# Optimization experiments

Hardware: AMD Instinct MI355X
Metric: run time of the kernel (lower is better)

The kernel has to match this reference:

```python
import jax, jax.numpy as jnp
import numpy as np

# dims: P planes, N planar nodes/plane, M nexus nodes, E edges/plane, C classes
P, N, M, E, C, FP, FN = 3, 100000, 30000, 200000, 5, 64, 32


def class_linear(x, W, b):
    # x: [..., C, in], W: [C, out, in], b: [C, out] -> [..., C, out]
    return jnp.einsum('...ci,coi->...co', x, W) + b


def setup_inputs() -> dict:
    key = jax.random.key(0)
    ks = jax.random.split(key, 12)
    def nrm(k, shape, scale=1.0):
        return jax.random.normal(k, shape, jnp.float32) * scale
    return {
        'x': nrm(ks[0], (P, N, C, FP)),
        'nexus': nrm(ks[1], (M, C, FN)),
        'edge_src': jax.random.randint(ks[2], (P, E), 0, N, jnp.int32),
        'edge_dst': jax.random.randint(ks[3], (P, E), 0, M, jnp.int32),
        'Wn1': nrm(ks[4], (C, FN, P * FP), (P * FP) ** -0.5),
        'bn1': jnp.zeros((C, FN), jnp.float32),
        'Wn2': nrm(ks[5], (C, FN, FN), FN ** -0.5),
        'bn2': jnp.zeros((C, FN), jnp.float32),
        'We': nrm(ks[6], (P, C, 1, FP + FN), (FP + FN) ** -0.5),
        'be': jnp.zeros((P, C, 1), jnp.float32),
        'Wd1': nrm(ks[7], (P, C, FP, FP + FN), (FP + FN) ** -0.5),
        'bd1': jnp.zeros((P, C, FP), jnp.float32),
        'Wd2': nrm(ks[8], (P, C, FP, FP), FP ** -0.5),
        'bd2': jnp.zeros((P, C, FP), jnp.float32),
    }


def reference(x, nexus, edge_src, edge_dst, Wn1, bn1, Wn2, bn2,
              We, be, Wd1, bd1, Wd2, bd2):
    # --- nexus_up: SimpleConv (sum-aggregate planar features at nexus nodes) ---
    def up_one(xp, src, dst):
        return jax.ops.segment_sum(xp[src], dst, num_segments=M)  # [M,C,FP]
    up = jax.vmap(up_one)(x, edge_src, edge_dst)                   # [P,M,C,FP]
    # torch.cat(n, dim=-1) over planes -> [M, C, P*FP]
    n_cat = jnp.transpose(up, (1, 2, 0, 3)).reshape(M, C, P * FP)

    # --- nexus_net: ClassLinear -> tanh -> ClassLinear -> tanh ---
    n = jnp.tanh(class_linear(n_cat, Wn1, bn1))
    n = jnp.tanh(class_linear(n, Wn2, bn2))                        # [M,C,FN]

    # --- nexus_down per plane (flow target_to_source, aggr mean at src) ---
    def down_one(xp, src, dst, We_p, be_p, W1, b1, W2, b2):
        x_i = xp[src]                                              # [E,C,FP]
        n_j = n[dst]                                               # [E,C,FN]
        feat = jax.lax.stop_gradient(jnp.concatenate([x_i, n_j], -1))
        # per-class scalar logit, softmax over class dim (dim=1)
        w = jax.nn.softmax(class_linear(feat, We_p, be_p), axis=1)  # [E,C,1]
        msg = w * n_j                                               # [E,C,FN]
        s = jax.ops.segment_sum(msg, src, num_segments=N)           # [N,C,FN]
        cnt = jax.ops.segment_sum(jnp.ones((E,), msg.dtype), src, num_segments=N)
        aggr = s / jnp.maximum(cnt, 1.0)[:, None, None]             # scatter-mean
        h = jnp.tanh(class_linear(jnp.concatenate([xp, aggr], -1), W1, b1))
        return jnp.tanh(class_linear(h, W2, b2))                    # [N,C,FP]

    out = jax.vmap(down_one)(x, edge_src, edge_dst, We, be, Wd1, bd1, Wd2, bd2)
    return out  # [P,N,C,FP] updated planar embeddings (x['u'],x['v'],x['y'])
```

## Files before the change

kernel.cpp:

```cpp
#include <hip/hip_runtime.h>
#include <hip/hip_fp16.h>

#define P_ 3
#define N_ 100000
#define M_ 30000
#define E_ 200000
#define C_ 5
#define FP_ 64
#define FN_ 32
#define PFP_ 192
#define FPFN_ 96
#define PE_ 600000
#define PN_ 300000
#define PM_ 90000
#define NT_ 64
#define TILES_ ((N_ + NT_ - 1) / NT_)
#define NTD_ 128
#define TILESD_ ((N_ + NTD_ - 1) / NTD_)
#define CFN_ 160
#define NW1_ 92160
#define NW2_ 61440
#define NWN1_ 30720
#define NB_S_ ((PN_ + 1023) / 1024)
#define NB_D_ ((PM_ + 1023) / 1024)
#define NB_CNT_ ((PE_ + 255) / 256)
#define NB_WC_ ((NW1_ + 255) / 256)
#define NB_PROJ_ (P_ * TILES_)
#define NB_FILL_ ((PE_ + 255) / 256)

typedef _Float16 f16x8 __attribute__((ext_vector_type(8)));
typedef float f32x4 __attribute__((ext_vector_type(4)));

__device__ __forceinline__ float fast_tanh(float v) {
  float t = __expf(2.0f * v);
  return 1.0f - __fdividef(2.0f, t + 1.0f);
}

__device__ __forceinline__ f16x8 ld8(const __half* p) {
  return *(const f16x8*)(const void*)p;
}

__global__ void k_countw(const int* __restrict__ esrc, const int* __restrict__ edst,
                         int* __restrict__ cnt_src, int* __restrict__ cnt_dst,
                         const float* __restrict__ Wd1, const float* __restrict__ Wd2,
                         const float* __restrict__ Wn1,
                         __half* __restrict__ w1h, __half* __restrict__ w2h,
                         __half* __restrict__ wn1h) {
  int b = blockIdx.x;
  if (b < NB_CNT_) {
    int i = b * 256 + threadIdx.x;
    if (i >= PE_) return;
    int p = i / E_;
    atomicAdd(&cnt_src[p * N_ + esrc[i]], 1);
    atomicAdd(&cnt_dst[p * M_ + edst[i]], 1);
  } else {
    int i = (b - NB_CNT_) * 256 + threadIdx.x;
    if (i < NW1_) w1h[i] = __float2half(Wd1[i]);
    if (i < NW2_) w2h[i] = __float2half(Wd2[i]);
    if (i < NWN1_) wn1h[i] = __float2half(Wn1[i]);
  }
}

__global__ void k_scan1c(const int* __restrict__ in_s, int* __restrict__ out_s,
                         int* __restrict__ aux_s,
                         const int* __restrict__ in_d, int* __restrict__ out_d,
                         int* __restrict__ aux_d) {
  __shared__ int lds[256];
  int b = blockIdx.x, t = threadIdx.x;
  const int* in;
  int* out;
  int* aux;
  int n;
  if (b < NB_S_) { in = in_s; out = out_s; aux = aux_s; n = PN_; }
  else           { b -= NB_S_; in = in_d; out = out_d; aux = aux_d; n = PM_; }
  int base = b * 1024 + t * 4;
  int v0 = (base + 0 < n) ? in[base + 0] : 0;
  int v1 = (base + 1 < n) ? in[base + 1] : 0;
  int v2 = (base + 2 < n) ? in[base + 2] : 0;
  int v3 = (base + 3 < n) ? in[base + 3] : 0;
  lds[t] = v0 + v1 + v2 + v3;
  __syncthreads();
  for (int off = 1; off < 256; off <<= 1) {
    int xv = (t >= off) ? lds[t - off] : 0;
    __syncthreads();
    lds[t] += xv;
    __syncthreads();
  }
  if (t == 255) aux[b] = lds[255];
  int run = (t == 0) ? 0 : lds[t - 1];
  if (base + 0 < n) out[base + 0] = run; run += v0;
  if (base + 1 < n) out[base + 1] = run; run += v1;
  if (base + 2 < n) out[base + 2] = run; run += v2;
  if (base + 3 < n) out[base + 3] = run;
}

__global__ void k_scan2c(int* __restrict__ aux_s, int* __restrict__ end_s,
                         int* __restrict__ aux_d, int* __restrict__ end_d) {
  __shared__ int lds[1024];
  int t = threadIdx.x;
  int* aux = (blockIdx.x == 0) ? aux_s : aux_d;
  int* offe = (blockIdx.x == 0) ? end_s : end_d;
  int nb = (blockIdx.x == 0) ? NB_S_ : NB_D_;
  lds[t] = (t < nb) ? aux[t] : 0;
  __syncthreads();
  for (int off = 1; off < 1024; off <<= 1) {
    int xv = (t >= off) ? lds[t - off] : 0;
    __syncthreads();
    lds[t] += xv;
    __syncthreads();
  }
  if (t < nb) aux[t] = (t == 0) ? 0 : lds[t - 1];
  if (t == 0) offe[0] = lds[nb - 1];
}

__global__ void k_scan3c(int* __restrict__ off_s, const int* __restrict__ aux_s,
                         int* __restrict__ cur_s,
                         int* __restrict__ off_d, const int* __restrict__ aux_d,
                         int* __restrict__ cur_d) {
  int i = blockIdx.x * 256 + threadIdx.x;
  if (i < PN_) {
    int v = off_s[i] + aux_s[i >> 10];
    off_s[i] = v;
    cur_s[i] = v;
  } else if (i < PN_ + PM_) {
    int j = i - PN_;
    int v = off_d[j] + aux_d[j >> 10];
    off_d[j] = v;
    cur_d[j] = v;
  }
}

__global__ __launch_bounds__(256) void k_projfill(
    const float* __restrict__ x, const __half* __restrict__ wn1h,
    const float* __restrict__ We,
    __half* __restrict__ y, float* __restrict__ xdot,
    __half* __restrict__ xh, int write_xh,
    const int* __restrict__ esrc, const int* __restrict__ edst,
    int* __restrict__ cur_src, int* __restrict__ cur_dst,
    int* __restrict__ list_src, int* __restrict__ list_src_e,
    int* __restrict__ list_dst, int* __restrict__ list_dst_e) {
  __shared__ __align__(16) __half xs[NT_ * 320];
  int bp = blockIdx.x;
  int t = threadIdx.x;

  if (bp >= NB_PROJ_) {
    int i = (bp - NB_PROJ_) * 256 + t;
    if (i < PE_) {
      int p = i / E_;
      int s = esrc[i], d = edst[i];
      int ps = atomicAdd(&cur_src[p * N_ + s], 1);
      list_src[ps] = d;
      list_src_e[ps] = i;
      int pd = atomicAdd(&cur_dst[p * M_ + d], 1);
      list_dst[pd] = s;
      list_dst_e[pd] = i;
    }
    return;
  }

  int p = bp / TILES_, tile = bp % TILES_;
  int base = tile * NT_;
  int rows = min(NT_, N_ - base);

  const float* xb = x + (size_t)(p * N_ + base) * 320;
  __half* xo = xh + (size_t)(p * N_ + base) * 320;
  for (int idx = t; idx < rows * 40; idx += 256) {
    int row = idx / 40, col = idx % 40;
    const float4* s4 = (const float4*)&xb[row * 320 + col * 8];
    float4 v0 = s4[0], v1 = s4[1];
    union { __half2 h[4]; float4 f; } u4;
    u4.h[0] = __floats2half2_rn(v0.x, v0.y);
    u4.h[1] = __floats2half2_rn(v0.z, v0.w);
    u4.h[2] = __floats2half2_rn(v1.x, v1.y);
    u4.h[3] = __floats2half2_rn(v1.z, v1.w);
    *(float4*)&xs[row * 320 + ((col * 8) ^ ((row & 7) << 3))] = u4.f;
    if (write_xh) *(float4*)&xo[row * 320 + col * 8] = u4.f;
  }
  __syncthreads();

  int w = t >> 6, l = t & 63;
  int l15 = l & 15, l4 = l >> 4;
  int nA = w * 16 + l15;
  int swzA = (nA & 7) << 3;

  #pragma unroll
  for (int c = 0; c < C_; ++c) {
    f16x8 a0 = ld8(&xs[nA * 320 + ((c * 64 + 0  + l4 * 8) ^ swzA)]);
    f16x8 a1 = ld8(&xs[nA * 320 + ((c * 64 + 32 + l4 * 8) ^ swzA)]);
    #pragma unroll
    for (int ct = 0; ct < 2; ++ct) {
      const __half* wb = &wn1h[(size_t)(c * 32 + ct * 16 + l15) * PFP_ + p * 64];
      f16x8 b0 = ld8(&wb[0  + l4 * 8]);
      f16x8 b1 = ld8(&wb[32 + l4 * 8]);
      f32x4 acc = (f32x4){0.f, 0.f, 0.f, 0.f};
      acc = __builtin_amdgcn_mfma_f32_16x16x32_f16(a0, b0, acc, 0, 0, 0);
      acc = __builtin_amdgcn_mfma_f32_16x16x32_f16(a1, b1, acc, 0, 0, 0);
      #pragma unroll
      for (int r = 0; r < 4; ++r) {
        int node = w * 16 + l4 * 4 + r;
        if (node < rows)
          y[(size_t)(p * N_ + base + node) * CFN_ + c * 32 + ct * 16 + l15] =
              __float2half(acc[r]);
      }
    }
  }

  for (int idx = t; idx < C_ * NT_; idx += 256) {
    int cx = idx >> 6, nodex = idx & 63;
    if (nodex < rows) {
      int swz = (nodex & 7) << 3;
      const float2* wer = (const float2*)&We[(p * C_ + cx) * FPFN_];
      float s = 0.f;
      #pragma unroll
      for (int i = 0; i < 32; ++i) {
        __half2 xv = *(const __half2*)&xs[nodex * 320 + ((cx * 64 + 2 * i) ^ swz)];
        float2 wv = wer[i];
        s += __low2float(xv) * wv.x + __high2float(xv) * wv.y;
      }
      xdot[(size_t)(p * N_ + base + nodex) * C_ + cx] = s;
    }
  }
}

__global__ __launch_bounds__(320) void k_nexus(
    const __half* __restrict__ y,
    const int* __restrict__ off_dst, const int* __restrict__ list_dst,
    const int* __restrict__ list_dst_e, const int* __restrict__ esrc,
    const float* __restrict__ bn1,
    const float* __restrict__ Wn2, const float* __restrict__ bn2,
    const float* __restrict__ We,
    const float* __restrict__ xdot, const float* __restrict__ be,
    __half* __restrict__ nout, __half* __restrict__ wbuf) {
  __shared__ float part[4][CFN_];
  __shared__ __align__(16) float h1S[CFN_];
  __shared__ __align__(16) float h2S[CFN_];
  __shared__ float ndS[P_ * C_];
  __shared__ float beS[P_ * C_];
  int m = blockIdx.x;
  int t = threadIdx.x;
  int g = t / 80, u2 = t % 80;

  float afx = 0.f, afy = 0.f;
  #pragma unroll
  for (int p = 0; p < P_; ++p) {
    int o0 = off_dst[p * M_ + m];
    int o1 = off_dst[p * M_ + m + 1];
    const __half2* yp2 = (const __half2*)(y + (size_t)p * N_ * CFN_);
    for (int e0 = o0 + g; e0 < o1; e0 += 8) {
      int e1 = e0 + 4;
      int s0 = list_dst[e0];
      int s1 = list_dst[e1 < o1 ? e1 : e0];
      __half2 v0 = yp2[(size_t)s0 * 80 + u2];
      __half2 v1 = yp2[(size_t)s1 * 80 + u2];
      afx += __low2float(v0); afy += __high2float(v0);
      if (e1 < o1) { afx += __low2float(v1); afy += __high2float(v1); }
    }
  }
  part[g][2 * u2]     = afx;
  part[g][2 * u2 + 1] = afy;
  __syncthreads();
  if (t < CFN_) {
    float pre = part[0][t] + part[1][t] + part[2][t] + part[3][t] + bn1[t];
    h1S[t] = fast_tanh(pre);
  }
  __syncthreads();
  if (t < CFN_) {
    int c = t >> 5;
    const float4* f4 = (const float4*)&h1S[c * FN_];
    const float4* w4 = (const float4*)&Wn2[(size_t)t * FN_];
    float a = bn2[t];
    #pragma unroll
    for (int i = 0; i < FN_ / 4; ++i) {
      float4 f = f4[i], wv = w4[i];
      a += f.x * wv.x + f.y * wv.y + f.z * wv.z + f.w * wv.w;
    }
    float nv = fast_tanh(a);
    h2S[t] = nv;
    nout[(size_t)m * CFN_ + t] = __float2half(nv);
  }
  __syncthreads();
  if (t < P_ * C_) {
    int p = t / C_, cc = t % C_;
    const float* wv = &We[(p * C_ + cc) * FPFN_ + FP_];
    float a = 0.f;
    #pragma unroll
    for (int j = 0; j < FN_; ++j) a += h2S[cc * FN_ + j] * wv[j];
    ndS[t] = a;
    beS[t] = be[t];
  }
  __syncthreads();
  #pragma unroll
  for (int p = 0; p < P_; ++p) {
    int o0 = off_dst[p * M_ + m];
    int o1 = off_dst[p * M_ + m + 1];
    for (int e = o0 + t; e < o1; e += 320) {
      int i = list_dst_e[e];
      int src = esrc[i];
      const float* xd = &xdot[(size_t)(p * N_ + src) * C_];
      float lg[C_];
      #pragma unroll
      for (int cc = 0; cc < C_; ++cc) lg[cc] = xd[cc] + ndS[p * C_ + cc] + beS[p * C_ + cc];
      float mx = fmaxf(fmaxf(fmaxf(lg[0], lg[1]), fmaxf(lg[2], lg[3])), lg[4]);
      float s = 0.f;
      #pragma unroll
      for (int cc = 0; cc < C_; ++cc) { lg[cc] = __expf(lg[cc] - mx); s += lg[cc]; }
      float inv = __fdividef(1.0f, s);
      __half* wp = &wbuf[(size_t)i * C_];
      #pragma unroll
      for (int cc = 0; cc < C_; ++cc) wp[cc] = __float2half(lg[cc] * inv);
    }
  }
}

template<int XH>
__global__ __launch_bounds__(256, 6) void k_dec(
    const float* __restrict__ x, const __half* __restrict__ xh,
    const __half* __restrict__ nout, const __half* __restrict__ wbuf,
    const int* __restrict__ off_src, const int* __restrict__ list_src,
    const int* __restrict__ list_src_e,
    const __half* __restrict__ w1h, const float* __restrict__ bd1,
    const __half* __restrict__ w2h, const float* __restrict__ bd2,
    float* __restrict__ out) {
  __shared__ __align__(16) __half featS[NTD_ * 104];

  int bp = blockIdx.x;
  int pc = bp / TILESD_;
  int tile = bp % TILESD_;
  int p = pc / C_, c = pc % C_;
  int base = tile * NTD_;
  int rows = min(NTD_, N_ - base);

  int t = threadIdx.x;
  int w = t >> 6, l = t & 63;
  int l15 = l & 15, l4 = l >> 4;

  if constexpr (XH) {
    for (int idx = t; idx < NTD_ * 8; idx += 256) {
      int node = idx >> 3, q = idx & 7;
      if (node < rows) {
        float4 v = *(const float4*)&xh[(size_t)(p * N_ + base + node) * 320 + c * 64 + q * 8];
        *(float4*)&featS[node * 104 + q * 8] = v;
      }
    }
  } else {
    for (int idx = t; idx < NTD_ * 16; idx += 256) {
      int node = idx >> 4, fq = idx & 15;
      if (node < rows) {
        float4 v = *(const float4*)&x[(size_t)(p * N_ + base + node) * 320 + c * 64 + fq * 4];
        __half2* dst = (__half2*)&featS[node * 104 + fq * 4];
        dst[0] = __floats2half2_rn(v.x, v.y);
        dst[1] = __floats2half2_rn(v.z, v.w);
      }
    }
  }
  {
    int nd = t >> 1, hf = t & 1;
    if (nd < rows) {
      int pn = p * N_ + base + nd;
      int o0 = off_src[pn], o1 = off_src[pn + 1];
      __half2 acc[8];
      #pragma unroll
      for (int i = 0; i < 8; ++i) acc[i] = __floats2half2_rn(0.f, 0.f);
      for (int e = o0; e < o1; e += 2) {
        int e1 = e + 1;
        bool has1 = (e1 < o1);
        int d0 = list_src[e];
        int i0 = list_src_e[e];
        int d1 = list_src[has1 ? e1 : e];
        int i1 = list_src_e[has1 ? e1 : e];
        __half wg0h = wbuf[(size_t)i0 * C_ + c];
        __half wg1h = wbuf[(size_t)i1 * C_ + c];
        const __half2* nr0 = (const __half2*)&nout[(size_t)d0 * CFN_ + c * FN_ + hf * 16];
        const __half2* nr1 = (const __half2*)&nout[(size_t)d1 * CFN_ + c * FN_ + hf * 16];
        __half2 v0[8], v1[8];
        #pragma unroll
        for (int i = 0; i < 8; ++i) v0[i] = nr0[i];
        #pragma unroll
        for (int i = 0; i < 8; ++i) v1[i] = nr1[i];
        __half2 wg0 = __half2half2(wg0h);
        #pragma unroll
        for (int i = 0; i < 8; ++i) acc[i] = __hfma2(wg0, v0[i], acc[i]);
        if (has1) {
          __half2 wg1 = __half2half2(wg1h);
          #pragma unroll
          for (int i = 0; i < 8; ++i) acc[i] = __hfma2(wg1, v1[i], acc[i]);
        }
      }
      float invd = __fdividef(1.0f, fmaxf((float)(o1 - o0), 1.0f));
      __half2 invd2 = __float2half2_rn(invd);
      __half2* dst2 = (__half2*)&featS[nd * 104 + 64 + hf * 16];
      #pragma unroll
      for (int i = 0; i < 8; ++i) dst2[i] = __hmul2(acc[i], invd2);
    }
  }
  __syncthreads();

  int rbase = w * 32;
  const __half* w1g = w1h + (size_t)(p * C_ + c) * 64 * 96;
  const __half* w2g = w2h + (size_t)(p * C_ + c) * 64 * 64;

  f32x4 acc[2][4];
  #pragma unroll
  for (int tt = 0; tt < 4; ++tt) {
    float bv = bd1[(p * C_ + c) * FP_ + tt * 16 + l15];
    #pragma unroll
    for (int rt = 0; rt < 2; ++rt) acc[rt][tt] = (f32x4){bv, bv, bv, bv};
  }
  #pragma unroll
  for (int s = 0; s < 3; ++s) {
    f16x8 a0 = ld8(&featS[(rbase + l15) * 104 + s * 32 + l4 * 8]);
    f16x8 a1 = ld8(&featS[(rbase + 16 + l15) * 104 + s * 32 + l4 * 8]);
    #pragma unroll
    for (int tt = 0; tt < 4; ++tt) {
      f16x8 b = ld8(&w1g[(tt * 16 + l15) * 96 + s * 32 + l4 * 8]);
      acc[0][tt] = __builtin_amdgcn_mfma_f32_16x16x32_f16(a0, b, acc[0][tt], 0, 0, 0);
      acc[1][tt] = __builtin_amdgcn_mfma_f32_16x16x32_f16(a1, b, acc[1][tt], 0, 0, 0);
    }
  }
  #pragma unroll
  for (int rt = 0; rt < 2; ++rt)
    #pragma unroll
    for (int tt = 0; tt < 4; ++tt) {
      #pragma unroll
      for (int r = 0; r < 4; ++r) {
        int nrow = rbase + rt * 16 + l4 * 4 + r;
        featS[nrow * 104 + tt * 16 + l15] = __float2half(fast_tanh(acc[rt][tt][r]));
      }
    }

  f32x4 acc2[2][4];
  #pragma unroll
  for (int tt = 0; tt < 4; ++tt) {
    float bv = bd2[(p * C_ + c) * FP_ + tt * 16 + l15];
    #pragma unroll
    for (int rt = 0; rt < 2; ++rt) acc2[rt][tt] = (f32x4){bv, bv, bv, bv};
  }
  #pragma unroll
  for (int s = 0; s < 2; ++s) {
    f16x8 a0 = ld8(&featS[(rbase + l15) * 104 + s * 32 + l4 * 8]);
    f16x8 a1 = ld8(&featS[(rbase + 16 + l15) * 104 + s * 32 + l4 * 8]);
    #pragma unroll
    for (int tt = 0; tt < 4; ++tt) {
      f16x8 b = ld8(&w2g[(tt * 16 + l15) * 64 + s * 32 + l4 * 8]);
      acc2[0][tt] = __builtin_amdgcn_mfma_f32_16x16x32_f16(a0, b, acc2[0][tt], 0, 0, 0);
      acc2[1][tt] = __builtin_amdgcn_mfma_f32_16x16x32_f16(a1, b, acc2[1][tt], 0, 0, 0);
    }
  }
  #pragma unroll
  for (int rt = 0; rt < 2; ++rt)
    #pragma unroll
    for (int tt = 0; tt < 4; ++tt) {
      #pragma unroll
      for (int r = 0; r < 4; ++r) {
        int nrow = rbase + rt * 16 + l4 * 4 + r;
        int node = base + nrow;
        if (node < N_) {
          out[(size_t)(p * N_ + node) * 320 + c * 64 + tt * 16 + l15] =
              fast_tanh(acc2[rt][tt][r]);
        }
      }
    }
}

#define WS_Y      0ll
#define WS_NOUT   24000000ll
#define WS_LISTSE 26400000ll
#define WS_WBUF   27000000ll
#define WS_XDOT   28800000ll
#define WS_OFFS   30750000ll
#define WS_OFFD   31050001ll
#define WS_CURS   31140002ll
#define WS_CURD   31440002ll
#define WS_LISTS  31530002ll
#define WS_LISTD  32130002ll
#define WS_AUX1   32730002ll
#define WS_AUX2   32730514ll
#define WS_W1H    32731026ll
#define WS_W2H    32777106ll
#define WS_LISTDE 32808000ll
#define WS_WN1H   33408000ll
#define WS_XH     33423360ll
#define WS_XH_END_BYTES ((WS_XH + 48000000ll) * 4ll)

extern "C" void kernel_launch(void* const* d_in, const int* in_sizes, int n_in,
                              void* d_out, int out_size, void* d_ws, size_t ws_size,
                              hipStream_t stream) {
  const float* x   = (const float*)d_in[0];
  const int* esrc  = (const int*)d_in[2];
  const int* edst  = (const int*)d_in[3];
  const float* Wn1 = (const float*)d_in[4];
  const float* bn1 = (const float*)d_in[5];
  const float* Wn2 = (const float*)d_in[6];
  const float* bn2 = (const float*)d_in[7];
  const float* We  = (const float*)d_in[8];
  const float* be  = (const float*)d_in[9];
  const float* Wd1 = (const float*)d_in[10];
  const float* bd1 = (const float*)d_in[11];
  const float* Wd2 = (const float*)d_in[12];
  const float* bd2 = (const float*)d_in[13];
  float* out = (float*)d_out;

  float* wsf = (float*)d_ws;
  int*   wsi = (int*)d_ws;
  __half* ybuf = (__half*)d_ws;
  __half* nout = (__half*)(wsi + WS_NOUT);
  __half* wbuf = (__half*)(wsi + WS_WBUF);
  float* xdot = wsf + WS_XDOT;
  int* off_src = wsi + WS_OFFS;
  int* off_dst = wsi + WS_OFFD;
  int* cur_src = wsi + WS_CURS;
  int* cur_dst = wsi + WS_CURD;
  int* list_src = wsi + WS_LISTS;
  int* list_src_e = wsi + WS_LISTSE;
  int* list_dst = wsi + WS_LISTD;
  int* list_dst_e = wsi + WS_LISTDE;
  int* aux1 = wsi + WS_AUX1;
  int* aux2 = wsi + WS_AUX2;
  __half* w1h = (__half*)(wsi + WS_W1H);
  __half* w2h = (__half*)(wsi + WS_W2H);
  __half* wn1h = (__half*)(wsi + WS_WN1H);
  __half* xh  = (__half*)(wsi + WS_XH);

  int use_xh = (ws_size >= (size_t)WS_XH_END_BYTES) ? 1 : 0;

  hipMemsetAsync(cur_src, 0, (PN_ + PM_) * sizeof(int), stream);
  k_countw<<<NB_CNT_ + NB_WC_, 256, 0, stream>>>(esrc, edst, cur_src, cur_dst,
                                                 Wd1, Wd2, Wn1, w1h, w2h, wn1h);
  k_scan1c<<<NB_S_ + NB_D_, 256, 0, stream>>>(cur_src, off_src, aux1,
                                              cur_dst, off_dst, aux2);
  k_scan2c<<<2, 1024, 0, stream>>>(aux1, off_src + PN_, aux2, off_dst + PM_);
  k_scan3c<<<(PN_ + PM_ + 255) / 256, 256, 0, stream>>>(off_src, aux1, cur_src,
                                                        off_dst, aux2, cur_dst);

  k_projfill<<<NB_PROJ_ + NB_FILL_, 256, 0, stream>>>(
      x, wn1h, We, ybuf, xdot, xh, use_xh,
      esrc, edst, cur_src, cur_dst,
      list_src, list_src_e, list_dst, list_dst_e);

  k_nexus<<<M_, 320, 0, stream>>>(ybuf, off_dst, list_dst, list_dst_e, esrc,
                                  bn1, Wn2, bn2, We, xdot, be, nout, wbuf);

  if (use_xh) {
    k_dec<1><<<P_ * C_ * TILESD_, 256, 0, stream>>>(x, xh, nout, wbuf,
                                                    off_src, list_src, list_src_e,
                                                    w1h, bd1, w2h, bd2, out);
  } else {
    k_dec<0><<<P_ * C_ * TILESD_, 256, 0, stream>>>(x, xh, nout, wbuf,
                                                    off_src, list_src, list_src_e,
                                                    w1h, bd1, w2h, bd2, out);
  }
}
```

Before: 783.2 us.

## Widen projfill blocks to 512 threads and vectorize nexus gather

k_projfill now runs 512 threads per block. The two column tiles of the MFMA projection are split across 8 waves instead of being looped inside 4 waves, and the edge-fill part covers 512 edges per block. k_nexus now gathers neighbor rows with 16-byte loads, so 20 threads cover a 160-half row and 16 edge groups run in parallel, reduced through a larger shared partial buffer. The aim is more parallelism and fewer, wider memory transactions on the gather. The cost is extra shared memory and more register accumulators per thread.

```diff
diff --git a/kernel.cpp b/kernel.cpp
--- a/kernel.cpp
+++ b/kernel.cpp
@@ -26,7 +26,7 @@
 #define NB_CNT_ ((PE_ + 255) / 256)
 #define NB_WC_ ((NW1_ + 255) / 256)
 #define NB_PROJ_ (P_ * TILES_)
-#define NB_FILL_ ((PE_ + 255) / 256)
+#define NB_FILL_ ((PE_ + 511) / 512)
 
 typedef _Float16 f16x8 __attribute__((ext_vector_type(8)));
 typedef float f32x4 __attribute__((ext_vector_type(4)));
@@ -130,7 +130,7 @@
   }
 }
 
-__global__ __launch_bounds__(256) void k_projfill(
+__global__ __launch_bounds__(512) void k_projfill(
     const float* __restrict__ x, const __half* __restrict__ wn1h,
     const float* __restrict__ We,
     __half* __restrict__ y, float* __restrict__ xdot,
@@ -144,7 +144,7 @@
   int t = threadIdx.x;
 
   if (bp >= NB_PROJ_) {
-    int i = (bp - NB_PROJ_) * 256 + t;
+    int i = (bp - NB_PROJ_) * 512 + t;
     if (i < PE_) {
       int p = i / E_;
       int s = esrc[i], d = edst[i];
@@ -164,7 +164,7 @@
 
   const float* xb = x + (size_t)(p * N_ + base) * 320;
   __half* xo = xh + (size_t)(p * N_ + base) * 320;
-  for (int idx = t; idx < rows * 40; idx += 256) {
+  for (int idx = t; idx < rows * 40; idx += 512) {
     int row = idx / 40, col = idx % 40;
     const float4* s4 = (const float4*)&xb[row * 320 + col * 8];
     float4 v0 = s4[0], v1 = s4[1];
@@ -180,32 +180,30 @@
 
   int w = t >> 6, l = t & 63;
   int l15 = l & 15, l4 = l >> 4;
-  int nA = w * 16 + l15;
+  int q4 = w & 3, ct = w >> 2;
+  int nA = q4 * 16 + l15;
   int swzA = (nA & 7) << 3;
 
   #pragma unroll
   for (int c = 0; c < C_; ++c) {
     f16x8 a0 = ld8(&xs[nA * 320 + ((c * 64 + 0  + l4 * 8) ^ swzA)]);
     f16x8 a1 = ld8(&xs[nA * 320 + ((c * 64 + 32 + l4 * 8) ^ swzA)]);
-    #pragma unroll
-    for (int ct = 0; ct < 2; ++ct) {
-      const __half* wb = &wn1h[(size_t)(c * 32 + ct * 16 + l15) * PFP_ + p * 64];
-      f16x8 b0 = ld8(&wb[0  + l4 * 8]);
-      f16x8 b1 = ld8(&wb[32 + l4 * 8]);
-      f32x4 acc = (f32x4){0.f, 0.f, 0.f, 0.f};
-      acc = __builtin_amdgcn_mfma_f32_16x16x32_f16(a0, b0, acc, 0, 0, 0);
-      acc = __builtin_amdgcn_mfma_f32_16x16x32_f16(a1, b1, acc, 0, 0, 0);
-      #pragma unroll
-      for (int r = 0; r < 4; ++r) {
-        int node = w * 16 + l4 * 4 + r;
-        if (node < rows)
-          y[(size_t)(p * N_ + base + node) * CFN_ + c * 32 + ct * 16 + l15] =
-              __float2half(acc[r]);
-      }
-    }
-  }
-
-  for (int idx = t; idx < C_ * NT_; idx += 256) {
+    const __half* wb = &wn1h[(size_t)(c * 32 + ct * 16 + l15) * PFP_ + p * 64];
+    f16x8 b0 = ld8(&wb[0  + l4 * 8]);
+    f16x8 b1 = ld8(&wb[32 + l4 * 8]);
+    f32x4 acc = (f32x4){0.f, 0.f, 0.f, 0.f};
+    acc = __builtin_amdgcn_mfma_f32_16x16x32_f16(a0, b0, acc, 0, 0, 0);
+    acc = __builtin_amdgcn_mfma_f32_16x16x32_f16(a1, b1, acc, 0, 0, 0);
+    #pragma unroll
+    for (int r = 0; r < 4; ++r) {
+      int node = q4 * 16 + l4 * 4 + r;
+      if (node < rows)
+        y[(size_t)(p * N_ + base + node) * CFN_ + c * 32 + ct * 16 + l15] =
+            __float2half(acc[r]);
+    }
+  }
+
+  for (int idx = t; idx < C_ * NT_; idx += 512) {
     int cx = idx >> 6, nodex = idx & 63;
     if (nodex < rows) {
       int swz = (nodex & 7) << 3;
@@ -231,36 +229,42 @@
     const float* __restrict__ We,
     const float* __restrict__ xdot, const float* __restrict__ be,
     __half* __restrict__ nout, __half* __restrict__ wbuf) {
-  __shared__ float part[4][CFN_];
+  __shared__ float part[16][CFN_];
   __shared__ __align__(16) float h1S[CFN_];
   __shared__ __align__(16) float h2S[CFN_];
   __shared__ float ndS[P_ * C_];
   __shared__ float beS[P_ * C_];
   int m = blockIdx.x;
   int t = threadIdx.x;
-  int g = t / 80, u2 = t % 80;
-
-  float afx = 0.f, afy = 0.f;
+  int g = t / 20, u4 = t % 20;
+
+  float acc[8];
+  #pragma unroll
+  for (int i = 0; i < 8; ++i) acc[i] = 0.f;
   #pragma unroll
   for (int p = 0; p < P_; ++p) {
     int o0 = off_dst[p * M_ + m];
     int o1 = off_dst[p * M_ + m + 1];
-    const __half2* yp2 = (const __half2*)(y + (size_t)p * N_ * CFN_);
-    for (int e0 = o0 + g; e0 < o1; e0 += 8) {
-      int e1 = e0 + 4;
-      int s0 = list_dst[e0];
-      int s1 = list_dst[e1 < o1 ? e1 : e0];
-      __half2 v0 = yp2[(size_t)s0 * 80 + u2];
-      __half2 v1 = yp2[(size_t)s1 * 80 + u2];
-      afx += __low2float(v0); afy += __high2float(v0);
-      if (e1 < o1) { afx += __low2float(v1); afy += __high2float(v1); }
-    }
-  }
-  part[g][2 * u2]     = afx;
-  part[g][2 * u2 + 1] = afy;
+    const __half* yp = y + (size_t)p * N_ * CFN_;
+    for (int e = o0 + g; e < o1; e += 16) {
+      int s0 = list_dst[e];
+      float4 v = *(const float4*)&yp[(size_t)s0 * CFN_ + u4 * 8];
+      union { float4 f; __half2 h[4]; } uu;
+      uu.f = v;
+      #pragma unroll
+      for (int i = 0; i < 4; ++i) {
+        acc[2 * i]     += __low2float(uu.h[i]);
+        acc[2 * i + 1] += __high2float(uu.h[i]);
+      }
+    }
+  }
+  #pragma unroll
+  for (int i = 0; i < 8; ++i) part[g][u4 * 8 + i] = acc[i];
   __syncthreads();
   if (t < CFN_) {
-    float pre = part[0][t] + part[1][t] + part[2][t] + part[3][t] + bn1[t];
+    float pre = bn1[t];
+    #pragma unroll
+    for (int gg = 0; gg < 16; ++gg) pre += part[gg][t];
     h1S[t] = fast_tanh(pre);
   }
   __syncthreads();
@@ -532,7 +536,7 @@
   k_scan3c<<<(PN_ + PM_ + 255) / 256, 256, 0, stream>>>(off_src, aux1, cur_src,
                                                         off_dst, aux2, cur_dst);
 
-  k_projfill<<<NB_PROJ_ + NB_FILL_, 256, 0, stream>>>(
+  k_projfill<<<NB_PROJ_ + NB_FILL_, 512, 0, stream>>>(
       x, wn1h, We, ybuf, xdot, xh, use_xh,
       esrc, edst, cur_src, cur_dst,
       list_src, list_src_e, list_dst, list_dst_e);
```

After: 718.5 us. 8.3% less time.
